# Performance work log

Measured on AMD Instinct MI355X. Metric: run time of the kernel, lower is better.

The kernel has to match this reference:

```python
import jax, jax.numpy as jnp
import numpy as np

B, S, C = 2, 2048, 2048
N, D = 16, 128          # heads, head_dim
DH = D // 2             # complex half dim = 64
F, H, W = 8, 16, 16     # f_p*h_p*w_p == S
MAX_ROPE = 1024
EPS = 1e-6


def setup_inputs() -> dict:
    key = jax.random.key(0)
    ks = jax.random.split(key, 8)
    # RoPE frequencies as unit complex numbers stored as (cos, sin) pairs.
    t_dim = DH - 2 * (DH // 3)  # 22
    s_dim = DH // 3             # 21
    pos = jnp.arange(MAX_ROPE, dtype=jnp.float32)
    def block(d):
        inv = 1.0 / (10000.0 ** (jnp.arange(d, dtype=jnp.float32) / d))
        return pos[:, None] * inv[None, :]
    ang = jnp.concatenate([block(t_dim), block(s_dim), block(s_dim)], axis=1)  # [MAX_ROPE, DH]
    freqs_cs = jnp.stack([jnp.cos(ang), jnp.sin(ang)], axis=-1).astype(jnp.float32)
    w_scale = 0.02
    return {
        "x": jax.random.normal(ks[0], (B, S, C), jnp.float32),
        "freqs_cs": freqs_cs,
        "wq": jax.random.normal(ks[1], (C, C), jnp.float32) * w_scale,
        "bq": jnp.zeros((C,), jnp.float32),
        "wk": jax.random.normal(ks[2], (C, C), jnp.float32) * w_scale,
        "bk": jnp.zeros((C,), jnp.float32),
        "wv": jax.random.normal(ks[3], (C, C), jnp.float32) * w_scale,
        "bv": jnp.zeros((C,), jnp.float32),
        "wo": jax.random.normal(ks[4], (C, C), jnp.float32) * w_scale,
        "bo": jnp.zeros((C,), jnp.float32),
        "gq": jnp.ones((C,), jnp.float32),
        "gk": jnp.ones((C,), jnp.float32),
        "frame_mask": jnp.ones((B, S), dtype=bool),
        "f_p": F, "h_p": H, "w_p": W,
    }


def _rmsnorm(t, g, eps=EPS):
    return t * jax.lax.rsqrt(jnp.mean(t * t, axis=-1, keepdims=True) + eps) * g


def _rope_volume(freqs_cs, f_p, h_p, w_p):
    # Build per-token (cos, sin) over the 3D grid, matching split/narrow/expand/cat.
    t_dim = DH - 2 * (DH // 3)
    s_dim = DH // 3
    def vol(a):  # a: [MAX_ROPE, DH] -> [S, DH]
        at = jnp.broadcast_to(a[:f_p, None, None, :t_dim], (f_p, h_p, w_p, t_dim))
        ah = jnp.broadcast_to(a[None, :h_p, None, t_dim:t_dim + s_dim], (f_p, h_p, w_p, s_dim))
        aw = jnp.broadcast_to(a[None, None, :w_p, t_dim + s_dim:], (f_p, h_p, w_p, s_dim))
        return jnp.concatenate([at, ah, aw], axis=-1).reshape(f_p * h_p * w_p, DH)
    return vol(freqs_cs[..., 0]), vol(freqs_cs[..., 1])


def _apply_rope(x, cos, sin):
    # x: [B, S, N, D]; complex multiply on interleaved (real, imag) pairs.
    b, s, n, d = x.shape
    xr, xi = x.reshape(b, s, n, DH, 2)[..., 0], x.reshape(b, s, n, DH, 2)[..., 1]
    c = cos[None, :, None, :]
    sn = sin[None, :, None, :]
    out = jnp.stack([xr * c - xi * sn, xr * sn + xi * c], axis=-1)
    return out.reshape(b, s, n, d)


def reference(x, freqs_cs, wq, bq, wk, bk, wv, bv, wo, bo, gq, gk, frame_mask, f_p, h_p, w_p):
    b, s = x.shape[:2]
    m = frame_mask[..., None]  # [B, S, 1]
    q = jnp.where(m, x @ wq.T + bq, 0.0)
    k = jnp.where(m, x @ wk.T + bk, 0.0)
    v = jnp.where(m, x @ wv.T + bv, 0.0)
    q = _rmsnorm(q, gq).reshape(b, s, N, D)
    k = _rmsnorm(k, gk).reshape(b, s, N, D)
    v = v.reshape(b, s, N, D)
    cos, sin = _rope_volume(freqs_cs, f_p, h_p, w_p)
    q = _apply_rope(q, cos, sin)
    k = _apply_rope(k, cos, sin)
    scale = 1.0 / jnp.sqrt(jnp.float32(D))
    scores = jnp.einsum("bqnd,bknd->bnqk", q, k) * scale
    bias = jnp.where(frame_mask[:, None, None, :], 0.0, -1e9).astype(scores.dtype)
    p = jax.nn.softmax(scores + bias, axis=-1)
    out = jnp.einsum("bnqk,bknd->bqnd", p, v)
    out = jnp.where(frame_mask[:, :, None, None], out, 0.0)
    out = out.reshape(b, s, N * D)
    out = out @ wo.T + bo
    return jnp.where(m, out, 0.0)
```

## Files before the change

kernel.cpp:

```cpp
#include <hip/hip_runtime.h>
#include <hip/hip_bf16.h>
#include <stdint.h>


#define S_LEN 2048
#define C_DIM 2048
#define NH    16
#define HD    128

typedef __attribute__((ext_vector_type(8))) short short8;
typedef __attribute__((ext_vector_type(4))) short short4v;
typedef __attribute__((ext_vector_type(4))) float f32x4;
typedef __attribute__((ext_vector_type(2))) unsigned uint2v;

__device__ __forceinline__ short f2bf(float f) {
  union { float f; unsigned u; } a; a.f = f;
  unsigned u = a.u;
  return (short)((u + 0x7fffu + ((u >> 16) & 1u)) >> 16);
}
__device__ __forceinline__ float bf2f(short s) {
  union { float f; unsigned u; } a; a.u = ((unsigned)(unsigned short)s) << 16;
  return a.f;
}

#if defined(__has_builtin)
#if __has_builtin(__builtin_amdgcn_cvt_pk_bf16_f32)
#define HAVE_PK_BF16 1
#endif
#endif
__device__ __forceinline__ unsigned pk_bf16(float a, float b) {
#ifdef HAVE_PK_BF16
  typedef __attribute__((ext_vector_type(2))) __bf16 bf16x2;
  bf16x2 r = __builtin_amdgcn_cvt_pk_bf16_f32(a, b);
  union { bf16x2 v; unsigned u; } c; c.v = r; return c.u;
#else
  return (unsigned)(unsigned short)f2bf(a) | ((unsigned)(unsigned short)f2bf(b) << 16);
#endif
}

__device__ __forceinline__ void gload16(const short* g, short* l) {
  __builtin_amdgcn_global_load_lds((const __attribute__((address_space(1))) void*)g,
                                   (__attribute__((address_space(3))) void*)l,
                                   16, 0, 0);
}

__global__ __launch_bounds__(256) void cvt_bf16(const float* __restrict__ in,
                                                short* __restrict__ out, int n8) {
  int i = blockIdx.x * 256 + threadIdx.x;
  if (i >= n8) return;
  const float4* p = (const float4*)(in + (size_t)i * 8);
  float4 v0 = p[0], v1 = p[1];
  short8 o;
  o[0]=f2bf(v0.x); o[1]=f2bf(v0.y); o[2]=f2bf(v0.z); o[3]=f2bf(v0.w);
  o[4]=f2bf(v1.x); o[5]=f2bf(v1.y); o[6]=f2bf(v1.z); o[7]=f2bf(v1.w);
  *(short8*)(out + (size_t)i * 8) = o;
}

__global__ __launch_bounds__(256) void cvt_bf16_w4(const float* __restrict__ w0,
                                                   const float* __restrict__ w1,
                                                   const float* __restrict__ w2,
                                                   const float* __restrict__ w3,
                                                   short* o0, short* o1, short* o2, short* o3,
                                                   int n8) {
  int y = blockIdx.y;
  const float* in = y == 0 ? w0 : (y == 1 ? w1 : (y == 2 ? w2 : w3));
  short* out = y == 0 ? o0 : (y == 1 ? o1 : (y == 2 ? o2 : o3));
  int i = blockIdx.x * 256 + threadIdx.x;
  if (i >= n8) return;
  const float4* p = (const float4*)(in + (size_t)i * 8);
  float4 v0 = p[0], v1 = p[1];
  short8 o;
  o[0]=f2bf(v0.x); o[1]=f2bf(v0.y); o[2]=f2bf(v0.z); o[3]=f2bf(v0.w);
  o[4]=f2bf(v1.x); o[5]=f2bf(v1.y); o[6]=f2bf(v1.z); o[7]=f2bf(v1.w);
  *(short8*)(out + (size_t)i * 8) = o;
}

__global__ __launch_bounds__(512, 2) void gemm_qk(const short* __restrict__ A,
                                                  const short* __restrict__ Wq,
                                                  const short* __restrict__ Wk,
                                                  const float* __restrict__ bq,
                                                  const float* __restrict__ bk,
                                                  short* __restrict__ Oq,
                                                  short* __restrict__ Ok) {
  __shared__ __align__(16) short As[4 * 8192];
  __shared__ __align__(16) short Bs[4 * 8192];
  const int tid = threadIdx.x;
  const int w = tid >> 6, lane = tid & 63, quad = lane >> 4, l15 = lane & 15;
  const int wm = w >> 2, wn = w & 3;

  const int wg = blockIdx.x;
  const int swz = (wg & 7) * 32 + (wg >> 3);
  const int m0 = (swz & 15) << 8;
  const int yy = swz >> 4;
  const int mat = yy >> 3;
  const int n0 = (yy & 7) << 8;
  const short* Bw = mat == 0 ? Wq : Wk;
  const float* bias = mat == 0 ? bq : bk;

  f32x4 zero = {0.f, 0.f, 0.f, 0.f};
  f32x4 acc[8][4];
#pragma unroll
  for (int i = 0; i < 8; i++)
#pragma unroll
    for (int j = 0; j < 4; j++) acc[i][j] = zero;

  const int sub0 = w * 2, sub1 = w * 2 + 1;
  const int rowoff = lane >> 2;
  const int xoff = ((lane & 3) ^ ((lane >> 3) & 3)) * 8;
  const int offA0 = (m0 + sub0 * 16 + rowoff) * C_DIM + xoff;
  const int offA1 = (m0 + sub1 * 16 + rowoff) * C_DIM + xoff;
  const int offB0 = (n0 + sub0 * 16 + rowoff) * C_DIM + xoff;
  const int offB1 = (n0 + sub1 * 16 + rowoff) * C_DIM + xoff;
  const int cp = (quad ^ ((l15 >> 1) & 3)) * 8;
  const int laneA = (wm * 128 + l15) * 32 + cp;
  const int laneB = (wn * 64 + l15) * 32 + cp;

  short8 afrag[4], bfrag[4];

#define BARX do { asm volatile("" ::: "memory"); __builtin_amdgcn_s_barrier(); \
                  asm volatile("" ::: "memory"); } while (0)
#define STAGE_A(slot, s) do { \
    gload16(A + offA0 + (s) * 32, &As[(slot) * 8192 + sub0 * 512]); \
    gload16(A + offA1 + (s) * 32, &As[(slot) * 8192 + sub1 * 512]); } while (0)
#define STAGE_B(slot, s) do { \
    gload16(Bw + offB0 + (s) * 32, &Bs[(slot) * 8192 + sub0 * 512]); \
    gload16(Bw + offB1 + (s) * 32, &Bs[(slot) * 8192 + sub1 * 512]); } while (0)
#define LOAD_A(slot, MH) do { _Pragma("unroll") \
    for (int mf = 0; mf < 4; mf++) \
      afrag[mf] = *(const short8*)&As[(slot) * 8192 + laneA + ((MH) * 4 + mf) * 512]; } while (0)
#define LOAD_B(slot) do { _Pragma("unroll") \
    for (int nf = 0; nf < 4; nf++) \
      bfrag[nf] = *(const short8*)&Bs[(slot) * 8192 + laneB + nf * 512]; } while (0)
#define MFMA_H(MH) do { _Pragma("unroll") \
    for (int mf = 0; mf < 4; mf++) \
      _Pragma("unroll") \
      for (int nf = 0; nf < 4; nf++) \
        acc[(MH) * 4 + mf][nf] = __builtin_amdgcn_mfma_f32_16x16x32_bf16( \
            afrag[mf], bfrag[nf], acc[(MH) * 4 + mf][nf], 0, 0, 0); } while (0)

#define KTILE(p0, p1, sl3, t, DO3, DO4, DO5, VMC) do { \
    LOAD_A(p0, 0); LOAD_B(p0); \
    if (DO3) STAGE_A(sl3, 2 * (t) + 3); \
    BARX; __builtin_amdgcn_s_setprio(1); MFMA_H(0); __builtin_amdgcn_s_setprio(0); BARX; \
    LOAD_A(p0, 1); \
    if (DO4) STAGE_B(p0, 2 * (t) + 4); \
    BARX; __builtin_amdgcn_s_setprio(1); MFMA_H(1); __builtin_amdgcn_s_setprio(0); BARX; \
    LOAD_A(p1, 0); LOAD_B(p1); \
    if (DO4) STAGE_A(p0, 2 * (t) + 4); \
    BARX; __builtin_amdgcn_s_setprio(1); MFMA_H(0); __builtin_amdgcn_s_setprio(0); BARX; \
    LOAD_A(p1, 1); \
    if (DO5) STAGE_B(p1, 2 * (t) + 5); \
    BARX; __builtin_amdgcn_s_setprio(1); MFMA_H(1); __builtin_amdgcn_s_setprio(0); \
    asm volatile("s_waitcnt vmcnt(" #VMC ")" ::: "memory"); BARX; \
  } while (0)

  STAGE_A(0, 0); STAGE_B(0, 0);
  STAGE_A(1, 1); STAGE_B(1, 1);
  STAGE_B(2, 2); STAGE_A(2, 2); STAGE_B(3, 3);
  asm volatile("s_waitcnt vmcnt(6)" ::: "memory");
  BARX;

  for (int t = 0; t < 30; t += 2) {
    KTILE(0, 1, 3, t,     1, 1, 1, 6);
    KTILE(2, 3, 1, t + 1, 1, 1, 1, 6);
  }
  KTILE(0, 1, 3, 30, 1, 0, 0, 0);
  KTILE(2, 3, 1, 31, 0, 0, 0, 0);

#undef KTILE
#undef MFMA_H
#undef LOAD_B
#undef LOAD_A
#undef STAGE_B
#undef STAGE_A
#undef BARX

  short* Oc = mat == 0 ? Oq : Ok;
#pragma unroll
  for (int nf = 0; nf < 4; nf++) {
    int col = n0 + wn * 64 + nf * 16 + l15;
    float bv2 = bias[col];
#pragma unroll
    for (int mf = 0; mf < 8; mf++)
#pragma unroll
      for (int r = 0; r < 4; r++) {
        int rowi = m0 + wm * 128 + mf * 16 + quad * 4 + r;
        Oc[(size_t)rowi * C_DIM + col] = f2bf(acc[mf][nf][r] + bv2);
      }
  }
}

__global__ __launch_bounds__(256) void gemm_v(const short* __restrict__ A,
                                              const short* __restrict__ Wv,
                                              const float* __restrict__ bv,
                                              short* __restrict__ Ovt) {
  __shared__ __align__(16) short As[128 * 64];
  __shared__ __align__(16) short Bs[128 * 64];
  const int tid = threadIdx.x;
  const int w = tid >> 6, lane = tid & 63, quad = lane >> 4, l15 = lane & 15;
  const int wm = w >> 1, wn = w & 1;
  const int m0 = blockIdx.x * 128;
  const int n0 = blockIdx.y * 128;

  f32x4 zero = {0.f, 0.f, 0.f, 0.f};
  f32x4 acc[4][4];
#pragma unroll
  for (int i = 0; i < 4; i++)
#pragma unroll
    for (int j = 0; j < 4; j++) acc[i][j] = zero;

  const int lrow = lane >> 3;
  const int lcol = (((lane & 7) ^ lrow) * 8);
  const int sw = (l15 & 7);
  for (int k0 = 0; k0 < C_DIM; k0 += 64) {
    __syncthreads();
#pragma unroll
    for (int t = 0; t < 4; t++) {
      int c = w * 4 + t;
      int row = c * 8 + lrow;
      gload16(A  + (size_t)(m0 + row) * C_DIM + k0 + lcol, &As[c * 512]);
      gload16(Wv + (size_t)(n0 + row) * C_DIM + k0 + lcol, &Bs[c * 512]);
    }
    __syncthreads();
#pragma unroll
    for (int kk = 0; kk < 64; kk += 32) {
      short8 af[4], bf[4];
#pragma unroll
      for (int i = 0; i < 4; i++)
        af[i] = *(const short8*)&As[(wm * 64 + i * 16 + l15) * 64 + ((((kk >> 3) + quad) ^ sw) << 3)];
#pragma unroll
      for (int j = 0; j < 4; j++)
        bf[j] = *(const short8*)&Bs[(wn * 64 + j * 16 + l15) * 64 + ((((kk >> 3) + quad) ^ sw) << 3)];
#pragma unroll
      for (int i = 0; i < 4; i++)
#pragma unroll
        for (int j = 0; j < 4; j++)
          acc[i][j] = __builtin_amdgcn_mfma_f32_16x16x32_bf16(af[i], bf[j], acc[i][j], 0, 0, 0);
    }
  }
  const int b = m0 >> 11, sb = (m0 & (S_LEN - 1)) + wm * 64;
#pragma unroll
  for (int j = 0; j < 4; j++) {
    int col = n0 + wn * 64 + j * 16 + l15;
    float bv2 = bv[col];
    int n = col >> 7, d = col & 127;
#pragma unroll
    for (int i = 0; i < 4; i++) {
      int s = sb + i * 16 + quad * 4;
      short4v o;
#pragma unroll
      for (int r = 0; r < 4; r++) o[r] = f2bf(acc[i][j][r] + bv2);
      *(short4v*)(Ovt + ((size_t)(b * NH + n) * HD + d) * S_LEN + s) = o;
    }
  }
}

__global__ __launch_bounds__(256) void gemm_nt(const short* __restrict__ A,
                                               const short* __restrict__ Bw,
                                               const float* __restrict__ bias,
                                               float* __restrict__ Cc,
                                               int M, int Nn, int K) {
  __shared__ __align__(16) short As[128 * 64];
  __shared__ __align__(16) short Bs[128 * 64];
  const int tid = threadIdx.x;
  const int w = tid >> 6, lane = tid & 63, quad = lane >> 4, l15 = lane & 15;
  const int wm = w >> 1, wn = w & 1;
  const int m0 = blockIdx.x * 128, n0 = blockIdx.y * 128;

  f32x4 zero = {0.f, 0.f, 0.f, 0.f};
  f32x4 acc[4][4];
#pragma unroll
  for (int i = 0; i < 4; i++)
#pragma unroll
    for (int j = 0; j < 4; j++) acc[i][j] = zero;

  const int lrow = lane >> 3;
  const int lcol = (((lane & 7) ^ lrow) * 8);
  const int sw = (l15 & 7);
  for (int k0 = 0; k0 < K; k0 += 64) {
    __syncthreads();
#pragma unroll
    for (int t = 0; t < 4; t++) {
      int c = w * 4 + t;
      int row = c * 8 + lrow;
      gload16(A  + (size_t)(m0 + row) * K + k0 + lcol, &As[c * 512]);
      gload16(Bw + (size_t)(n0 + row) * K + k0 + lcol, &Bs[c * 512]);
    }
    __syncthreads();
#pragma unroll
    for (int kk = 0; kk < 64; kk += 32) {
      short8 af[4], bf[4];
#pragma unroll
      for (int i = 0; i < 4; i++)
        af[i] = *(const short8*)&As[(wm * 64 + i * 16 + l15) * 64 + ((((kk >> 3) + quad) ^ sw) << 3)];
#pragma unroll
      for (int j = 0; j < 4; j++)
        bf[j] = *(const short8*)&Bs[(wn * 64 + j * 16 + l15) * 64 + ((((kk >> 3) + quad) ^ sw) << 3)];
#pragma unroll
      for (int i = 0; i < 4; i++)
#pragma unroll
        for (int j = 0; j < 4; j++)
          acc[i][j] = __builtin_amdgcn_mfma_f32_16x16x32_bf16(af[i], bf[j], acc[i][j], 0, 0, 0);
    }
  }
#pragma unroll
  for (int j = 0; j < 4; j++) {
    int col = n0 + wn * 64 + j * 16 + l15;
    float bv = bias[col];
#pragma unroll
    for (int i = 0; i < 4; i++)
#pragma unroll
      for (int r = 0; r < 4; r++) {
        int rowi = m0 + wm * 64 + i * 16 + quad * 4 + r;
        Cc[(size_t)rowi * Nn + col] = acc[i][j][r] + bv;
      }
  }
}

__global__ __launch_bounds__(256) void rmsrope(const short* __restrict__ qin,
                                               const short* __restrict__ kin,
                                               const float* __restrict__ gq,
                                               const float* __restrict__ gk,
                                               const float* __restrict__ freqs,
                                               short* __restrict__ qout,
                                               short* __restrict__ kout) {
  const int which = blockIdx.y;
  const short* in = which ? kin : qin;
  const float* g = which ? gk : gq;
  short* out = which ? kout : qout;
  const float outscale = which ? 1.0f : 0.08838834764831843f * 1.4426950408889634f;
  const int row = blockIdx.x;
  const int s = row & (S_LEN - 1);
  const short* rp = in + (size_t)row * C_DIM;
  const int tid = threadIdx.x;
  const int e0 = tid * 8;
  short8 sv = *(const short8*)(rp + e0);
  float a[8];
#pragma unroll
  for (int t = 0; t < 8; t++) a[t] = bf2f(sv[t]);
  float ps = 0.f;
#pragma unroll
  for (int t = 0; t < 8; t++) ps += a[t] * a[t];
#pragma unroll
  for (int m = 32; m >= 1; m >>= 1) ps += __shfl_xor(ps, m);
  __shared__ float red[4];
  if ((tid & 63) == 0) red[tid >> 6] = ps;
  __syncthreads();
  float tot = red[0] + red[1] + red[2] + red[3];
  float sc = rsqrtf(tot * (1.0f / 2048.0f) + 1e-6f) * outscale;
  float4 g0 = *(const float4*)(g + e0);
  float4 g1 = *(const float4*)(g + e0 + 4);
  float gg[8] = {g0.x, g0.y, g0.z, g0.w, g1.x, g1.y, g1.z, g1.w};
  const int f = s >> 8, h = (s >> 4) & 15, wv = s & 15;
  short8 o;
#pragma unroll
  for (int q2 = 0; q2 < 4; q2++) {
    int p = (tid & 15) * 4 + q2;
    int pos = p < 22 ? f : (p < 43 ? h : wv);
    float cc = freqs[(pos * 64 + p) * 2];
    float ss = freqs[(pos * 64 + p) * 2 + 1];
    float xr = a[2 * q2] * gg[2 * q2] * sc, xi = a[2 * q2 + 1] * gg[2 * q2 + 1] * sc;
    o[2 * q2]     = f2bf(xr * cc - xi * ss);
    o[2 * q2 + 1] = f2bf(xr * ss + xi * cc);
  }
  *(short8*)(out + (size_t)row * C_DIM + e0) = o;
}

__global__ __launch_bounds__(512, 4) void flash(const short* __restrict__ qb,
                                                const short* __restrict__ kb,
                                                const short* __restrict__ vt,
                                                short* __restrict__ ob) {
  __shared__ __align__(16) short Ks[32 * 512];
  __shared__ __align__(16) short Vs[32 * 512];
  __shared__ __align__(16) short Ps[128 * 64];
  const int tid = threadIdx.x;
  const int w = tid >> 6, lane = tid & 63, quad = lane >> 4, l15 = lane & 15;
  const int fb = blockIdx.x;
  const int xcd = fb & 7, idx = fb >> 3;
  const int bn = xcd * 4 + (idx & 3), b = bn >> 4, n = bn & 15;
  const int q0 = (idx >> 2) * 128;

  short8 qf[4];
#pragma unroll
  for (int kc = 0; kc < 4; kc++) {
    int rowq = q0 + w * 16 + l15;
    qf[kc] = *(const short8*)(qb + (size_t)(b * S_LEN + rowq) * C_DIM + n * HD + kc * 32 + quad * 8);
  }

  short8 onesf;
#pragma unroll
  for (int t = 0; t < 8; t++) onesf[t] = (l15 == 0) ? (short)0x3f80 : (short)0;

  f32x4 zero = {0.f, 0.f, 0.f, 0.f};
  f32x4 oa[9];
#pragma unroll
  for (int j = 0; j < 9; j++) oa[j] = zero;

#define STAGEK(kk0) do { _Pragma("unroll") \
    for (int kc = 0; kc < 4; kc++) \
      gload16(kb + (size_t)(b * S_LEN + (kk0) + w * 16 + l15) * C_DIM + n * HD + kc * 32 + quad * 8, \
              &Ks[(w * 4 + kc) * 512]); } while (0)
#define STAGEV(kk0) do { _Pragma("unroll") \
    for (int kc2 = 0; kc2 < 4; kc2++) \
      gload16(vt + (size_t)(bn * HD + w * 16 + l15) * S_LEN + (kk0) + kc2 * 32 + quad * 8, \
              &Vs[(w * 4 + kc2) * 512]); } while (0)

#define QKSM(hh) do { \
    f32x4 sa[4]; \
    _Pragma("unroll") for (int jp = 0; jp < 4; jp++) sa[jp] = zero; \
    _Pragma("unroll") \
    for (int kc = 0; kc < 4; kc++) { \
      short8 kf[4]; \
      _Pragma("unroll") for (int jp = 0; jp < 4; jp++) \
        kf[jp] = *(const short8*)&Ks[(((hh) * 4 + jp) * 4 + kc) * 512 + lane * 8]; \
      __builtin_amdgcn_s_setprio(1); \
      _Pragma("unroll") for (int jp = 0; jp < 4; jp++) \
        sa[jp] = __builtin_amdgcn_mfma_f32_16x16x32_bf16(kf[jp], qf[kc], sa[jp], 0, 0, 0); \
      __builtin_amdgcn_s_setprio(0); \
    } \
    { \
      int m = w * 16 + l15; \
      _Pragma("unroll") \
      for (int jp = 0; jp < 4; jp++) { \
        uint2v pw; \
        pw[0] = pk_bf16(exp2f(sa[jp][0]), exp2f(sa[jp][1])); \
        pw[1] = pk_bf16(exp2f(sa[jp][2]), exp2f(sa[jp][3])); \
        int gw = (jp * 4 + quad) ^ ((l15 & 7) << 1); \
        *(uint2v*)&Ps[m * 64 + gw * 4] = pw; \
      } \
    } } while (0)

#define PVH(hh) do { \
    _Pragma("unroll") \
    for (int kc2p = 0; kc2p < 2; kc2p++) { \
      int kc2 = (hh) * 2 + kc2p; \
      short8 pf, vf2[8]; \
      { \
        int m = w * 16 + l15; \
        int g0 = (kc2p * 8 + quad * 2) ^ ((l15 & 7) << 1); \
        pf = *(const short8*)&Ps[m * 64 + g0 * 4]; \
      } \
      _Pragma("unroll") for (int jd = 0; jd < 8; jd++) \
        vf2[jd] = *(const short8*)&Vs[(jd * 4 + kc2) * 512 + lane * 8]; \
      __builtin_amdgcn_s_setprio(1); \
      _Pragma("unroll") for (int jd = 0; jd < 8; jd++) \
        oa[jd] = __builtin_amdgcn_mfma_f32_16x16x32_bf16(pf, vf2[jd], oa[jd], 0, 0, 0); \
      oa[8] = __builtin_amdgcn_mfma_f32_16x16x32_bf16(pf, onesf, oa[8], 0, 0, 0); \
      __builtin_amdgcn_s_setprio(0); \
    } } while (0)

  STAGEK(0);
  for (int k0 = 0; k0 < S_LEN; k0 += 128) {
    __syncthreads();
    STAGEV(k0);
    QKSM(0);
    __syncthreads();
    PVH(0);
    QKSM(1);
    __syncthreads();
    if (k0 + 128 < S_LEN) STAGEK(k0 + 128);
    PVH(1);
  }

#undef PVH
#undef QKSM
#undef STAGEV
#undef STAGEK

  {
    float inv[4];
#pragma unroll
    for (int r = 0; r < 4; r++) {
      float lr = __shfl(oa[8][r], lane & 48);
      inv[r] = 1.0f / lr;
    }
#pragma unroll
    for (int j = 0; j < 8; j++)
#pragma unroll
      for (int r = 0; r < 4; r++) {
        int rowq = q0 + w * 16 + quad * 4 + r;
        ob[(size_t)(b * S_LEN + rowq) * C_DIM + n * HD + j * 16 + l15] = f2bf(oa[j][r] * inv[r]);
      }
  }
}

extern "C" void kernel_launch(void* const* d_in, const int* in_sizes, int n_in,
                              void* d_out, int out_size, void* d_ws, size_t ws_size,
                              hipStream_t stream) {
  const float* x     = (const float*)d_in[0];
  const float* freqs = (const float*)d_in[1];
  const float* wq = (const float*)d_in[2];  const float* bq = (const float*)d_in[3];
  const float* wk = (const float*)d_in[4];  const float* bk = (const float*)d_in[5];
  const float* wv = (const float*)d_in[6];  const float* bv = (const float*)d_in[7];
  const float* wo = (const float*)d_in[8];  const float* bo = (const float*)d_in[9];
  const float* gq = (const float*)d_in[10]; const float* gk = (const float*)d_in[11];
  float* out = (float*)d_out;

  const size_t MS = 4096 * 2048;
  const size_t WS = 2048 * 2048;
  short* xb  = (short*)d_ws;
  short* wqb = xb + MS;
  short* wkb = wqb + WS;
  short* wvb = wkb + WS;
  short* wob = wvb + WS;
  short* q16 = wob + WS;
  short* k16 = q16 + MS;
  short* qbb = k16 + MS;
  short* kbb = qbb + MS;
  short* vtb = kbb + MS;
  short* obb = vtb + MS;

  cvt_bf16<<<dim3((int)(MS / 8 / 256)), dim3(256), 0, stream>>>(x, xb, (int)(MS / 8));
  cvt_bf16_w4<<<dim3((int)(WS / 8 / 256), 4), dim3(256), 0, stream>>>(
      wq, wk, wv, wo, wqb, wkb, wvb, wob, (int)(WS / 8));

  gemm_qk<<<dim3(256), dim3(512), 0, stream>>>(xb, wqb, wkb, bq, bk, q16, k16);
  gemm_v<<<dim3(32, 16), dim3(256), 0, stream>>>(xb, wvb, bv, vtb);

  rmsrope<<<dim3(4096, 2), dim3(256), 0, stream>>>(q16, k16, gq, gk, freqs, qbb, kbb);

  flash<<<dim3(512), dim3(512), 0, stream>>>(qbb, kbb, vtb, obb);

  gemm_nt<<<dim3(32, 16), dim3(256), 0, stream>>>(obb, wob, bo, out, 4096, 2048, 2048);
}
```

Baseline: 439.9 us.

## Redistribute softmax probabilities in registers via permlane swaps instead of LDS

The P tile no longer goes through LDS. The exp2'd scores are packed to bf16 and rearranged into the MFMA A-operand layout using v_permlane32_swap and v_permlane16_swap, then kept in registers. This removes the P LDS buffer, its writes and reads, and one __syncthreads per iteration. The loop is also restructured so both QK halves finish before all four PV chunks run. In exchange, more probabilities stay live in registers, which raises VGPR pressure at 512 threads with 4 waves per SIMD, and the QK/PV interleaving changes.

```diff
diff --git a/kernel.cpp b/kernel.cpp
--- a/kernel.cpp
+++ b/kernel.cpp
@@ -11,7 +11,6 @@
 typedef __attribute__((ext_vector_type(8))) short short8;
 typedef __attribute__((ext_vector_type(4))) short short4v;
 typedef __attribute__((ext_vector_type(4))) float f32x4;
-typedef __attribute__((ext_vector_type(2))) unsigned uint2v;
 
 __device__ __forceinline__ short f2bf(float f) {
   union { float f; unsigned u; } a; a.f = f;
@@ -36,6 +35,13 @@
 #else
   return (unsigned)(unsigned short)f2bf(a) | ((unsigned)(unsigned short)f2bf(b) << 16);
 #endif
+}
+
+__device__ __forceinline__ void p32swap(unsigned &a, unsigned &b) {
+  asm volatile("v_permlane32_swap_b32 %0, %1" : "+v"(a), "+v"(b));
+}
+__device__ __forceinline__ void p16swap(unsigned &a, unsigned &b) {
+  asm volatile("v_permlane16_swap_b32 %0, %1" : "+v"(a), "+v"(b));
 }
 
 __device__ __forceinline__ void gload16(const short* g, short* l) {
@@ -372,7 +378,6 @@
                                                 short* __restrict__ ob) {
   __shared__ __align__(16) short Ks[32 * 512];
   __shared__ __align__(16) short Vs[32 * 512];
-  __shared__ __align__(16) short Ps[128 * 64];
   const int tid = threadIdx.x;
   const int w = tid >> 6, lane = tid & 63, quad = lane >> 4, l15 = lane & 15;
   const int fb = blockIdx.x;
@@ -395,6 +400,9 @@
   f32x4 oa[9];
 #pragma unroll
   for (int j = 0; j < 9; j++) oa[j] = zero;
+
+  union pun { unsigned u[4]; short8 s; };
+  pun pa[4];
 
 #define STAGEK(kk0) do { _Pragma("unroll") \
     for (int kc = 0; kc < 4; kc++) \
@@ -418,51 +426,45 @@
         sa[jp] = __builtin_amdgcn_mfma_f32_16x16x32_bf16(kf[jp], qf[kc], sa[jp], 0, 0, 0); \
       __builtin_amdgcn_s_setprio(0); \
     } \
-    { \
-      int m = w * 16 + l15; \
+    _Pragma("unroll") \
+    for (int jp = 0; jp < 4; jp++) \
       _Pragma("unroll") \
-      for (int jp = 0; jp < 4; jp++) { \
-        uint2v pw; \
-        pw[0] = pk_bf16(exp2f(sa[jp][0]), exp2f(sa[jp][1])); \
-        pw[1] = pk_bf16(exp2f(sa[jp][2]), exp2f(sa[jp][3])); \
-        int gw = (jp * 4 + quad) ^ ((l15 & 7) << 1); \
-        *(uint2v*)&Ps[m * 64 + gw * 4] = pw; \
-      } \
-    } } while (0)
-
-#define PVH(hh) do { \
+      for (int r = 0; r < 4; r++) sa[jp][r] = exp2f(sa[jp][r]); \
     _Pragma("unroll") \
     for (int kc2p = 0; kc2p < 2; kc2p++) { \
-      int kc2 = (hh) * 2 + kc2p; \
-      short8 pf, vf2[8]; \
-      { \
-        int m = w * 16 + l15; \
-        int g0 = (kc2p * 8 + quad * 2) ^ ((l15 & 7) << 1); \
-        pf = *(const short8*)&Ps[m * 64 + g0 * 4]; \
-      } \
-      _Pragma("unroll") for (int jd = 0; jd < 8; jd++) \
-        vf2[jd] = *(const short8*)&Vs[(jd * 4 + kc2) * 512 + lane * 8]; \
-      __builtin_amdgcn_s_setprio(1); \
-      _Pragma("unroll") for (int jd = 0; jd < 8; jd++) \
-        oa[jd] = __builtin_amdgcn_mfma_f32_16x16x32_bf16(pf, vf2[jd], oa[jd], 0, 0, 0); \
-      oa[8] = __builtin_amdgcn_mfma_f32_16x16x32_bf16(pf, onesf, oa[8], 0, 0, 0); \
-      __builtin_amdgcn_s_setprio(0); \
+      unsigned w0 = pk_bf16(sa[kc2p * 2][0], sa[kc2p * 2][1]); \
+      unsigned w1 = pk_bf16(sa[kc2p * 2][2], sa[kc2p * 2][3]); \
+      unsigned w2 = pk_bf16(sa[kc2p * 2 + 1][0], sa[kc2p * 2 + 1][1]); \
+      unsigned w3 = pk_bf16(sa[kc2p * 2 + 1][2], sa[kc2p * 2 + 1][3]); \
+      p32swap(w0, w2); p16swap(w0, w2);   \
+      p32swap(w1, w3); p16swap(w1, w3);   \
+      pa[(hh) * 2 + kc2p].u[0] = w0; pa[(hh) * 2 + kc2p].u[1] = w1; \
+      pa[(hh) * 2 + kc2p].u[2] = w2; pa[(hh) * 2 + kc2p].u[3] = w3; \
     } } while (0)
+
+#define PVC(kc2) do { \
+    short8 vf2[8]; \
+    _Pragma("unroll") for (int jd = 0; jd < 8; jd++) \
+      vf2[jd] = *(const short8*)&Vs[(jd * 4 + (kc2)) * 512 + lane * 8]; \
+    __builtin_amdgcn_s_setprio(1); \
+    _Pragma("unroll") for (int jd = 0; jd < 8; jd++) \
+      oa[jd] = __builtin_amdgcn_mfma_f32_16x16x32_bf16(pa[kc2].s, vf2[jd], oa[jd], 0, 0, 0); \
+    oa[8] = __builtin_amdgcn_mfma_f32_16x16x32_bf16(pa[kc2].s, onesf, oa[8], 0, 0, 0); \
+    __builtin_amdgcn_s_setprio(0); \
+  } while (0)
 
   STAGEK(0);
   for (int k0 = 0; k0 < S_LEN; k0 += 128) {
     __syncthreads();
     STAGEV(k0);
     QKSM(0);
-    __syncthreads();
-    PVH(0);
     QKSM(1);
     __syncthreads();
     if (k0 + 128 < S_LEN) STAGEK(k0 + 128);
-    PVH(1);
-  }
-
-#undef PVH
+    PVC(0); PVC(1); PVC(2); PVC(3);
+  }
+
+#undef PVC
 #undef QKSM
 #undef STAGEV
 #undef STAGEK
```

Result: no change. 433.5 us (-1.5%).
